# Performance work log

Measured on AMD Instinct MI355X. Metric: run time of the kernel, lower is better.

Reference implementation:

```python
import jax, jax.numpy as jnp
import numpy as np

LAMDA = 1.0


def setup_inputs() -> dict:
    key = jax.random.key(0)
    k1, k2, k3, k4 = jax.random.split(key, 4)
    B, C, D = 16384, 1000, 512
    logits = jax.random.normal(k1, (B, C), dtype=jnp.float32)
    labels = jax.random.randint(k2, (B,), 0, C, dtype=jnp.int64)
    features = jax.random.normal(k3, (B, D), dtype=jnp.float32)
    global_protos = jax.random.normal(k4, (C, D), dtype=jnp.float32)
    return {"logits": logits, "labels": labels, "features": features,
            "global_protos": global_protos}


def reference(logits, labels, features, global_protos):
    # --- classification loss: mean cross-entropy ---
    logp = jax.nn.log_softmax(logits, axis=-1)                 # [B, C]
    ce_loss = -jnp.take_along_axis(logp, labels[:, None], axis=1).mean()
    ce_loss = jnp.where(jnp.isfinite(ce_loss), ce_loss, 0.0)

    # --- prototype alignment loss ---
    # Every label has a (finite) global prototype, so the per-sample dict
    # loop reduces to: gather proto by label, per-sample MSE, mean over B.
    gathered = global_protos[labels]                           # [B, D]
    per_sample_mse = jnp.mean((features - gathered) ** 2, axis=-1)  # [B]
    proto_loss = per_sample_mse.mean()

    total_loss = ce_loss + LAMDA * proto_loss
    total_loss = jnp.where(jnp.isfinite(total_loss), total_loss, ce_loss)
    return (total_loss, ce_loss, proto_loss)
```

## Files before the change

### kernel.cpp

```cpp
#include <hip/hip_runtime.h>
#include <math.h>


#ifndef INFINITY
#define INFINITY __builtin_inff()
#endif

__device__ __forceinline__ float safe_exp(float dm) {
    return __expf(fminf(dm, 0.0f));
}

__global__ __launch_bounds__(256) void fedtgp_rows(
    const float* __restrict__ logits,
    const int*   __restrict__ labels,
    const float* __restrict__ features,
    const float* __restrict__ protos,
    double* __restrict__ ce_part,
    double* __restrict__ pl_part,
    int B, int C, int D)
{
    const int tid  = threadIdx.x;
    const int lane = tid & 63;
    const int wv   = tid >> 6;
    const int row  = blockIdx.x * 4 + wv;

    __shared__ double sc[4], sp[4];

    float ce_b = 0.f, pl_b = 0.f;
    bool valid = (row < B);

    if (valid) {
        const int   lab  = labels[row];
        const float* lrow = logits + (size_t)row * C;
        const int C4 = C >> 2;
        const int D4 = D >> 2;

        float m = -INFINITY;
        float s = 0.f;
        float q = 0.f;

        for (int base = 0; base < C4; base += 256) {
            const float4* l4 = (const float4*)lrow;
            float4 v[4];
            #pragma unroll
            for (int k = 0; k < 4; ++k) {
                const int idx = base + lane + 64 * k;
                v[k] = (idx < C4) ? l4[idx]
                                  : make_float4(-INFINITY, -INFINITY, -INFINITY, -INFINITY);
            }
            float cm = m;
            #pragma unroll
            for (int k = 0; k < 4; ++k)
                cm = fmaxf(cm, fmaxf(fmaxf(v[k].x, v[k].y), fmaxf(v[k].z, v[k].w)));
            s *= safe_exp(m - cm);
            #pragma unroll
            for (int k = 0; k < 4; ++k) {
                s += safe_exp(v[k].x - cm) + safe_exp(v[k].y - cm)
                   + safe_exp(v[k].z - cm) + safe_exp(v[k].w - cm);
            }
            m = cm;
        }
        for (int c = (C4 << 2) + lane; c < C; c += 64) {
            const float x  = lrow[c];
            const float cm = fmaxf(m, x);
            s = s * safe_exp(m - cm) + safe_exp(x - cm);
            m = cm;
        }

        {
            const float4* f4 = (const float4*)(features + (size_t)row * D);
            const float4* p4 = (const float4*)(protos   + (size_t)lab * D);
            #pragma unroll
            for (int k = 0; k < 2; ++k) {
                const int idx = lane + 64 * k;
                float4 f = make_float4(0.f, 0.f, 0.f, 0.f);
                float4 p = make_float4(0.f, 0.f, 0.f, 0.f);
                if (idx < D4) { f = f4[idx]; p = p4[idx]; }
                const float dx = f.x - p.x, dy = f.y - p.y;
                const float dz = f.z - p.z, dw = f.w - p.w;
                q += dx * dx + dy * dy + dz * dz + dw * dw;
            }
            for (int idx = lane + 128; idx < D4; idx += 64) {
                const float4 f = f4[idx];
                const float4 p = p4[idx];
                const float dx = f.x - p.x, dy = f.y - p.y;
                const float dz = f.z - p.z, dw = f.w - p.w;
                q += dx * dx + dy * dy + dz * dz + dw * dw;
            }
            for (int d = (D4 << 2) + lane; d < D; d += 64) {
                const float df = features[(size_t)row * D + d]
                               - protos[(size_t)lab * D + d];
                q += df * df;
            }
        }

        #pragma unroll
        for (int off = 32; off > 0; off >>= 1) {
            const float om = __shfl_xor(m, off, 64);
            const float os = __shfl_xor(s, off, 64);
            q += __shfl_xor(q, off, 64);
            const float nm = fmaxf(m, om);
            s = s * safe_exp(m - nm) + os * safe_exp(om - nm);
            m = nm;
        }

        const float ll  = lrow[lab];
        const float lse = m + __logf(s);
        ce_b = lse - ll;
        pl_b = q / (float)D;
    }

    if (lane == 0) {
        sc[wv] = valid ? (double)ce_b : 0.0;
        sp[wv] = valid ? (double)pl_b : 0.0;
    }
    __syncthreads();
    if (tid == 0) {
        ce_part[blockIdx.x] = sc[0] + sc[1] + sc[2] + sc[3];
        pl_part[blockIdx.x] = sp[0] + sp[1] + sp[2] + sp[3];
    }
}

__global__ __launch_bounds__(1024) void fedtgp_finalize(
    const double* __restrict__ ce_part,
    const double* __restrict__ pl_part,
    float* __restrict__ out,
    int npart, double invB)
{
    const int tid  = threadIdx.x;
    const int lane = tid & 63;
    const int wv   = tid >> 6;
    __shared__ double rc[16];
    __shared__ double rp[16];

    double c = 0.0, p = 0.0;
    for (int i = tid; i < npart; i += 1024) {
        c += ce_part[i];
        p += pl_part[i];
    }
    #pragma unroll
    for (int off = 32; off > 0; off >>= 1) {
        c += __shfl_xor(c, off, 64);
        p += __shfl_xor(p, off, 64);
    }
    if (lane == 0) { rc[wv] = c; rp[wv] = p; }
    __syncthreads();

    if (tid == 0) {
        double cs = 0.0, ps = 0.0;
        #pragma unroll
        for (int k = 0; k < 16; ++k) { cs += rc[k]; ps += rp[k]; }
        float ce = (float)(cs * invB);
        float pl = (float)(ps * invB);
        if (!isfinite(ce)) ce = 0.0f;
        float tot = ce + pl;
        if (!isfinite(tot)) tot = ce;
        out[0] = tot;
        out[1] = ce;
        out[2] = pl;
    }
}

extern "C" void kernel_launch(void* const* d_in, const int* in_sizes, int n_in,
                              void* d_out, int out_size, void* d_ws, size_t ws_size,
                              hipStream_t stream)
{
    const float* logits   = (const float*)d_in[0];
    const int*   labels   = (const int*)  d_in[1];
    const float* features = (const float*)d_in[2];
    const float* protos   = (const float*)d_in[3];
    float* out = (float*)d_out;

    const int B = in_sizes[1];
    const int C = in_sizes[0] / B;
    const int D = in_sizes[2] / B;

    int nb = (B + 3) / 4;
    const size_t need_per_block = 2 * sizeof(double);
    if ((size_t)nb * need_per_block > ws_size) {
        nb = (int)(ws_size / need_per_block);
        if (nb < 1) nb = 1;
    }

    double* ce_part = (double*)d_ws;
    double* pl_part = ce_part + nb;

    fedtgp_rows<<<nb, 256, 0, stream>>>(logits, labels, features, protos,
                                        ce_part, pl_part, B, C, D);
    fedtgp_finalize<<<1, 1024, 0, stream>>>(ce_part, pl_part, out, nb,
                                            1.0 / (double)B);
}
```

Baseline: 121.8 us.

## Specialize single-pass row kernel with all loads issued upfront and per-row partials

Adds a fast path for C up to 1024 and D up to 512 where each wavefront issues all logit, feature and prototype float4 loads at once with clamped indices, then does a single max and a single exp-sum instead of an online-rescaled loop. The wave-level max is reduced first and each lane's sum is rescaled once. The shared-memory block reduction and __syncthreads are removed, and each row writes a float2 partial that the finalize kernel sums in double. This exposes more memory-level parallelism per wave, at the cost of more partials for the finalize kernel to read and a possible race-free early return for rows past B.

Result: no change. 122.1 us (+0.3%).

```diff
diff --git a/kernel.cpp b/kernel.cpp
--- a/kernel.cpp
+++ b/kernel.cpp
@@ -15,85 +15,104 @@
     const int*   __restrict__ labels,
     const float* __restrict__ features,
     const float* __restrict__ protos,
-    double* __restrict__ ce_part,
-    double* __restrict__ pl_part,
+    float2* __restrict__ part,
     int B, int C, int D)
 {
     const int tid  = threadIdx.x;
     const int lane = tid & 63;
     const int wv   = tid >> 6;
     const int row  = blockIdx.x * 4 + wv;
+    if (row >= B) return;
 
-    __shared__ double sc[4], sp[4];
+    const int lab = labels[row];
+    const int C4 = C >> 2;
+    const int D4 = D >> 2;
+    const float* lrow = logits + (size_t)row * C;
 
-    float ce_b = 0.f, pl_b = 0.f;
-    bool valid = (row < B);
+    float ce, pl;
 
-    if (valid) {
-        const int   lab  = labels[row];
-        const float* lrow = logits + (size_t)row * C;
-        const int C4 = C >> 2;
-        const int D4 = D >> 2;
+    if (C4 >= 64 && C4 <= 256 && D4 >= 64 && D4 <= 128 &&
+        (C & 3) == 0 && (D & 3) == 0) {
+        const float4* l4 = (const float4*)lrow;
+        const float4* f4 = (const float4*)(features + (size_t)row * D);
+        const float4* p4 = (const float4*)(protos   + (size_t)lab * D);
 
-        float m = -INFINITY;
-        float s = 0.f;
-        float q = 0.f;
+        const int i1 = min(lane + 64,  C4 - 1);
+        const int i2 = min(lane + 128, C4 - 1);
+        const int i3 = min(lane + 192, C4 - 1);
+        const int j1 = min(lane + 64,  D4 - 1);
 
-        for (int base = 0; base < C4; base += 256) {
-            const float4* l4 = (const float4*)lrow;
-            float4 v[4];
-            #pragma unroll
-            for (int k = 0; k < 4; ++k) {
-                const int idx = base + lane + 64 * k;
-                v[k] = (idx < C4) ? l4[idx]
-                                  : make_float4(-INFINITY, -INFINITY, -INFINITY, -INFINITY);
-            }
-            float cm = m;
-            #pragma unroll
-            for (int k = 0; k < 4; ++k)
-                cm = fmaxf(cm, fmaxf(fmaxf(v[k].x, v[k].y), fmaxf(v[k].z, v[k].w)));
-            s *= safe_exp(m - cm);
-            #pragma unroll
-            for (int k = 0; k < 4; ++k) {
-                s += safe_exp(v[k].x - cm) + safe_exp(v[k].y - cm)
-                   + safe_exp(v[k].z - cm) + safe_exp(v[k].w - cm);
-            }
-            m = cm;
+        float4 v0 = l4[lane];
+        float4 v1 = l4[i1];
+        float4 v2 = l4[i2];
+        float4 v3 = l4[i3];
+        float4 f0 = f4[lane];
+        float4 f1 = f4[j1];
+        float4 p0 = p4[lane];
+        float4 p1 = p4[j1];
+        const float ll = lrow[lab];
+
+        const bool b1 = (lane + 64  < C4);
+        const bool b2 = (lane + 128 < C4);
+        const bool b3 = (lane + 192 < C4);
+        const bool d1 = (lane + 64  < D4);
+        const float NI = -INFINITY;
+        v1.x = b1 ? v1.x : NI; v1.y = b1 ? v1.y : NI;
+        v1.z = b1 ? v1.z : NI; v1.w = b1 ? v1.w : NI;
+        v2.x = b2 ? v2.x : NI; v2.y = b2 ? v2.y : NI;
+        v2.z = b2 ? v2.z : NI; v2.w = b2 ? v2.w : NI;
+        v3.x = b3 ? v3.x : NI; v3.y = b3 ? v3.y : NI;
+        v3.z = b3 ? v3.z : NI; v3.w = b3 ? v3.w : NI;
+
+        float m = fmaxf(fmaxf(fmaxf(v0.x, v0.y), fmaxf(v0.z, v0.w)),
+                        fmaxf(fmaxf(v1.x, v1.y), fmaxf(v1.z, v1.w)));
+        m = fmaxf(m, fmaxf(fmaxf(v2.x, v2.y), fmaxf(v2.z, v2.w)));
+        m = fmaxf(m, fmaxf(fmaxf(v3.x, v3.y), fmaxf(v3.z, v3.w)));
+
+        float s = safe_exp(v0.x - m) + safe_exp(v0.y - m)
+                + safe_exp(v0.z - m) + safe_exp(v0.w - m);
+        s += safe_exp(v1.x - m) + safe_exp(v1.y - m)
+           + safe_exp(v1.z - m) + safe_exp(v1.w - m);
+        s += safe_exp(v2.x - m) + safe_exp(v2.y - m)
+           + safe_exp(v2.z - m) + safe_exp(v2.w - m);
+        s += safe_exp(v3.x - m) + safe_exp(v3.y - m)
+           + safe_exp(v3.z - m) + safe_exp(v3.w - m);
+
+        float dx = f0.x - p0.x, dy = f0.y - p0.y;
+        float dz = f0.z - p0.z, dw = f0.w - p0.w;
+        float q = dx * dx + dy * dy + dz * dz + dw * dw;
+        dx = f1.x - p1.x; dy = f1.y - p1.y;
+        dz = f1.z - p1.z; dw = f1.w - p1.w;
+        float q1 = dx * dx + dy * dy + dz * dz + dw * dw;
+        q += d1 ? q1 : 0.0f;
+
+        float M = m;
+        #pragma unroll
+        for (int off = 32; off > 0; off >>= 1)
+            M = fmaxf(M, __shfl_xor(M, off, 64));
+        s *= safe_exp(m - M);
+        #pragma unroll
+        for (int off = 32; off > 0; off >>= 1) {
+            s += __shfl_xor(s, off, 64);
+            q += __shfl_xor(q, off, 64);
         }
-        for (int c = (C4 << 2) + lane; c < C; c += 64) {
+
+        ce = (M + __logf(s)) - ll;
+        pl = q / (float)D;
+    } else {
+        float m = -INFINITY, s = 0.f, q = 0.f;
+        for (int c = lane; c < C; c += 64) {
             const float x  = lrow[c];
             const float cm = fmaxf(m, x);
             s = s * safe_exp(m - cm) + safe_exp(x - cm);
             m = cm;
         }
-
-        {
-            const float4* f4 = (const float4*)(features + (size_t)row * D);
-            const float4* p4 = (const float4*)(protos   + (size_t)lab * D);
-            #pragma unroll
-            for (int k = 0; k < 2; ++k) {
-                const int idx = lane + 64 * k;
-                float4 f = make_float4(0.f, 0.f, 0.f, 0.f);
-                float4 p = make_float4(0.f, 0.f, 0.f, 0.f);
-                if (idx < D4) { f = f4[idx]; p = p4[idx]; }
-                const float dx = f.x - p.x, dy = f.y - p.y;
-                const float dz = f.z - p.z, dw = f.w - p.w;
-                q += dx * dx + dy * dy + dz * dz + dw * dw;
-            }
-            for (int idx = lane + 128; idx < D4; idx += 64) {
-                const float4 f = f4[idx];
-                const float4 p = p4[idx];
-                const float dx = f.x - p.x, dy = f.y - p.y;
-                const float dz = f.z - p.z, dw = f.w - p.w;
-                q += dx * dx + dy * dy + dz * dz + dw * dw;
-            }
-            for (int d = (D4 << 2) + lane; d < D; d += 64) {
-                const float df = features[(size_t)row * D + d]
-                               - protos[(size_t)lab * D + d];
-                q += df * df;
-            }
+        for (int d = lane; d < D; d += 64) {
+            const float df = features[(size_t)row * D + d]
+                           - protos[(size_t)lab * D + d];
+            q += df * df;
         }
-
+        const float ll = lrow[lab];
         #pragma unroll
         for (int off = 32; off > 0; off >>= 1) {
             const float om = __shfl_xor(m, off, 64);
@@ -103,29 +122,17 @@
             s = s * safe_exp(m - nm) + os * safe_exp(om - nm);
             m = nm;
         }
-
-        const float ll  = lrow[lab];
-        const float lse = m + __logf(s);
-        ce_b = lse - ll;
-        pl_b = q / (float)D;
+        ce = (m + __logf(s)) - ll;
+        pl = q / (float)D;
     }
 
-    if (lane == 0) {
-        sc[wv] = valid ? (double)ce_b : 0.0;
-        sp[wv] = valid ? (double)pl_b : 0.0;
-    }
-    __syncthreads();
-    if (tid == 0) {
-        ce_part[blockIdx.x] = sc[0] + sc[1] + sc[2] + sc[3];
-        pl_part[blockIdx.x] = sp[0] + sp[1] + sp[2] + sp[3];
-    }
+    if (lane == 0) part[row] = make_float2(ce, pl);
 }
 
 __global__ __launch_bounds__(1024) void fedtgp_finalize(
-    const double* __restrict__ ce_part,
-    const double* __restrict__ pl_part,
+    const float2* __restrict__ part,
     float* __restrict__ out,
-    int npart, double invB)
+    int B, double invB)
 {
     const int tid  = threadIdx.x;
     const int lane = tid & 63;
@@ -134,9 +141,10 @@
     __shared__ double rp[16];
 
     double c = 0.0, p = 0.0;
-    for (int i = tid; i < npart; i += 1024) {
-        c += ce_part[i];
-        p += pl_part[i];
+    for (int i = tid; i < B; i += 1024) {
+        const float2 v = part[i];
+        c += (double)v.x;
+        p += (double)v.y;
     }
     #pragma unroll
     for (int off = 32; off > 0; off >>= 1) {
@@ -175,18 +183,10 @@
     const int C = in_sizes[0] / B;
     const int D = in_sizes[2] / B;
 
-    int nb = (B + 3) / 4;
-    const size_t need_per_block = 2 * sizeof(double);
-    if ((size_t)nb * need_per_block > ws_size) {
-        nb = (int)(ws_size / need_per_block);
-        if (nb < 1) nb = 1;
-    }
+    float2* part = (float2*)d_ws;
 
-    double* ce_part = (double*)d_ws;
-    double* pl_part = ce_part + nb;
-
+    const int nb = (B + 3) / 4;
     fedtgp_rows<<<nb, 256, 0, stream>>>(logits, labels, features, protos,
-                                        ce_part, pl_part, B, C, D);
-    fedtgp_finalize<<<1, 1024, 0, stream>>>(ce_part, pl_part, out, nb,
-                                            1.0 / (double)B);
+                                        part, B, C, D);
+    fedtgp_finalize<<<1, 1024, 0, stream>>>(part, out, B, 1.0 / (double)B);
 }
```
